# Optimization experiments

Measured on AMD Instinct MI355X. Metric: run time of the kernel, lower is better.

## Reference

```python
import jax, jax.numpy as jnp
import numpy as np

# Geometry constants (from init_kwargs)
H = 512            # volume rows
W = 512            # volume cols
N_ANGLES = 512     # number of projections
N_DET = 736        # detector bins (covers sqrt(2)*512 ~ 724 diagonal)
N_SAMP = 736       # integration samples along each ray
DET_SPACING = 1.0
STEP = 1.0         # ray sampling step (pixel units)


def _bilinear(img, px, py):
    """Bilinear interpolation of img[H,W] at float coords (px=col, py=row); zero outside."""
    x0 = jnp.floor(px)
    y0 = jnp.floor(py)
    fx = px - x0
    fy = py - y0
    x0i = x0.astype(jnp.int32)
    y0i = y0.astype(jnp.int32)

    def tap(yi, xi):
        valid = (xi >= 0) & (xi < W) & (yi >= 0) & (yi < H)
        v = img[jnp.clip(yi, 0, H - 1), jnp.clip(xi, 0, W - 1)]
        return jnp.where(valid, v, jnp.float32(0))

    v00 = tap(y0i, x0i)
    v01 = tap(y0i, x0i + 1)
    v10 = tap(y0i + 1, x0i)
    v11 = tap(y0i + 1, x0i + 1)
    return (v00 * (1 - fx) + v01 * fx) * (1 - fy) + (v10 * (1 - fx) + v11 * fx) * fy


def _parallel_projection2d(img, angles):
    """Parallel-beam Radon transform of img[H,W] -> sinogram [A, N_DET]."""
    cx = (W - 1) * 0.5
    cy = (H - 1) * 0.5
    # detector offsets s and ray-parameter samples t, centered
    s = (jnp.arange(N_DET, dtype=jnp.float32) - (N_DET - 1) * 0.5) * DET_SPACING
    t = (jnp.arange(N_SAMP, dtype=jnp.float32) - (N_SAMP - 1) * 0.5) * STEP

    def project_angle(theta):
        c = jnp.cos(theta)
        si = jnp.sin(theta)
        # ray point = s * (c, si) + t * (-si, c), shifted to image center. [D, T]
        px = s[:, None] * c - t[None, :] * si + cx
        py = s[:, None] * si + t[None, :] * c + cy
        return _bilinear(img, px, py).sum(axis=-1) * STEP  # [D]

    # sequential map over angles keeps intermediates at [D, T] instead of [A, D, T]
    return jax.lax.map(project_angle, angles)  # [A, D]


def setup_inputs() -> dict:
    key = jax.random.key(0)
    k1, k2 = jax.random.split(key)
    x = jax.random.normal(k1, (1, H, W), dtype=jnp.float32)
    # reco variable is constrained non-negative in the original (clip_by_value(x,0,inf))
    reco = jax.random.uniform(k2, (1, H, W), dtype=jnp.float32)
    angles = jnp.linspace(0.0, np.pi, N_ANGLES, endpoint=False, dtype=jnp.float32)
    return {"x": x, "reco": reco, "angles": angles}


def reference(x, reco, angles):
    updated_reco = x + reco                               # [1, H, W]
    sino = jax.vmap(lambda im: _parallel_projection2d(im, angles))(updated_reco)  # [1, A, D]
    return sino, reco
```

## Files before the change

### kernel.cpp

```cpp
#include <hip/hip_runtime.h>
#include <hip/hip_fp16.h>
#include <climits>


namespace {
constexpr int H = 512, W = 512, NA = 512, ND = 736, NS = 736;
constexpr int SINO_SIZE = NA * ND;
constexpr int IMG_SIZE = H * W;
constexpr int QN = 514;
constexpr int QS = 520;
constexpr int QUAD_SIZE = QN * QS;
constexpr int KSPLIT = 8;
}

typedef __fp16 h2 __attribute__((ext_vector_type(2)));
typedef float  f2 __attribute__((ext_vector_type(2)));

__global__ __launch_bounds__(256) void prep_quads(const float* __restrict__ x,
                                                  const float* __restrict__ reco,
                                                  uint2* __restrict__ Q,
                                                  uint2* __restrict__ QT,
                                                  float* __restrict__ reco_out,
                                                  float* __restrict__ sino) {
    __shared__ float tile[34][35];
    const int tx = threadIdx.x, ty = threadIdx.y;
    const int r0 = blockIdx.y * 32, c0 = blockIdx.x * 32;
    const int z  = blockIdx.z;

    if (z == 0) {
        const int nthr = 289 * 256;
        const int gtid = (blockIdx.y * 17 + blockIdx.x) * 256 + ty * 32 + tx;
        for (int i = gtid; i < SINO_SIZE; i += nthr) sino[i] = 0.f;
    }

    for (int li = ty * 32 + tx; li < 34 * 34; li += 256) {
        const int yy = li / 34, xx = li - yy * 34;
        const int r = r0 - 1 + yy, c = c0 - 1 + xx;
        float v = 0.f;
        if ((unsigned)r < 512u && (unsigned)c < 512u) {
            const int i = r * W + c;
            v = x[i] + reco[i];
        }
        tile[yy][xx] = v;
    }
    __syncthreads();

    const int t2 = ty + 8 * z;
    const int ri = r0 + t2, ci = c0 + tx;
    if (ri < QN && ci < QN) {
        uint2 q;
        q.x = __builtin_bit_cast(unsigned int,
              __builtin_amdgcn_cvt_pkrtz(tile[t2][tx],     tile[t2 + 1][tx]));
        q.y = __builtin_bit_cast(unsigned int,
              __builtin_amdgcn_cvt_pkrtz(tile[t2][tx + 1]     - tile[t2][tx],
                                         tile[t2 + 1][tx + 1] - tile[t2 + 1][tx]));
        Q[ri * QS + ci] = q;
    }
    const int ri2 = c0 + t2, ci2 = r0 + tx;
    if (ri2 < QN && ci2 < QN) {
        uint2 q;
        q.x = __builtin_bit_cast(unsigned int,
              __builtin_amdgcn_cvt_pkrtz(tile[tx][t2],     tile[tx][t2 + 1]));
        q.y = __builtin_bit_cast(unsigned int,
              __builtin_amdgcn_cvt_pkrtz(tile[tx + 1][t2]     - tile[tx][t2],
                                         tile[tx + 1][t2 + 1] - tile[tx][t2 + 1]));
        QT[ri2 * QS + ci2] = q;
    }
    const int rr = r0 + t2, cc = c0 + tx;
    if (rr < H && cc < W) reco_out[rr * W + cc] = reco[rr * W + cc];
}

__device__ inline void range1(float p0, float inc, float lo, float hi,
                              float& klo, float& khi) {
    if (inc > 1e-6f)       { klo = (lo - p0) / inc; khi = (hi - p0) / inc; }
    else if (inc < -1e-6f) { klo = (hi - p0) / inc; khi = (lo - p0) / inc; }
    else if (p0 >= lo && p0 <= hi) { klo = -1e9f; khi = 1e9f; }
    else                   { klo = 1e9f;  khi = -1e9f; }
}

__device__ __forceinline__ void samp_clamped(const uint2* __restrict__ base,
                                             float F1, float S1, float fi, float sl,
                                             int j, float& acc) {
    const float jf = (float)j;
    float pf = fmaf(jf, fi, F1);
    float ps = fmaf(jf, sl, S1);
    pf = fminf(fmaxf(pf, 0.f), 513.f);
    ps = fminf(fmaxf(ps, 0.f), 513.f);
    const float ff = floorf(pf), sf = floorf(ps);
    const float fx = pf - ff,   fy = ps - sf;
    const unsigned ai = (unsigned)fmaf(sf, 520.f, ff);
    const uint2 q = base[ai];
    const h2 l  = __builtin_bit_cast(h2, q.x);
    const h2 dl = __builtin_bit_cast(h2, q.y);
    const h2 fxx = __builtin_amdgcn_cvt_pkrtz(fx, fx);
    const h2 m = fxx * dl + l;
    const h2 wy = __builtin_amdgcn_cvt_pkrtz(1.f - fy, fy);
#if __has_builtin(__builtin_amdgcn_fdot2)
    acc = __builtin_amdgcn_fdot2(wy, m, acc, false);
#else
    acc += (float)wy.x * (float)m.x + (float)wy.y * (float)m.y;
#endif
}

__global__ __launch_bounds__(128) void proj_quad(const uint2* __restrict__ Q,
                                                 const uint2* __restrict__ QT,
                                                 const float* __restrict__ angles,
                                                 float* __restrict__ sino) {
    const int lane = threadIdx.x & 63;
    const int d = blockIdx.x * 128 + (threadIdx.x >> 6) * 64 + lane;
    const int a = blockIdx.y;
    const int z = blockIdx.z;

    float si, co;
    sincosf(angles[a], &si, &co);

    const float cx = (W - 1) * 0.5f, cy = (H - 1) * 0.5f;
    const float s  = (float)d - (ND - 1) * 0.5f;
    const float bx = fmaf(s, co, cx);
    const float by = fmaf(s, si, cy);

    const uint2* base;
    float f0, fi, s0, sl, dS;
    if (fabsf(co) >= fabsf(si)) { base = Q;  f0 = bx; fi = -si; s0 = by; sl = co;  dS = si; }
    else                        { base = QT; f0 = by; fi = co;  s0 = bx; sl = -si; dS = co; }

    const float t0 = -(float)(NS - 1) * 0.5f;
    float F0 = fmaf(t0, fi, f0);
    float S0 = fmaf(t0, sl, s0);
    if (sl < 0.f) {
        F0 = fmaf((float)(NS - 1), fi, F0); fi = -fi;
        S0 = fmaf((float)(NS - 1), sl, S0); sl = -sl;
    }

    float kloF, khiF, kloS, khiS;
    range1(F0, fi, -0.9999f, 511.9999f, kloF, khiF);
    range1(S0, sl, -0.9999f, 511.9999f, kloS, khiS);
    const int kA = max(0,      (int)ceilf(fmaxf(kloF, kloS)));
    const int kB = min(NS - 1, (int)floorf(fminf(khiF, khiS)));

    const int o = (int)rintf(-(float)lane * dS / sl);
    const float F1 = fmaf((float)o, fi, F0) + 1.f;
    const float S1 = fmaf((float)o, sl, S0) + 1.f;

    int jA, jB;
    if (kA <= kB) { jA = kA - o; jB = kB - o; }
    else          { jA = INT_MAX; jB = INT_MIN; }
    int Jlo = jA, Jhi = jB;
    #pragma unroll
    for (int off = 1; off < 64; off <<= 1) {
        Jlo = min(Jlo, __shfl_xor(Jlo, off));
        Jhi = max(Jhi, __shfl_xor(Jhi, off));
    }
    if (Jlo > Jhi) return;
    const int L  = Jhi - Jlo + 1;
    const int js = __builtin_amdgcn_readfirstlane(Jlo + (L * z) / KSPLIT);
    const int je = __builtin_amdgcn_readfirstlane(Jlo + (L * (z + 1)) / KSPLIT - 1);
    const int n  = je - js + 1;
    const int je2 = js + 2 * (n >> 1) - 1;

    const f2 fi2 = {fi, fi}, sl2 = {sl, sl};
    const f2 F12 = {F1, F1}, S12 = {S1, S1};
    const f2 c520 = {520.f, 520.f};
    f2 jf2 = {(float)js, (float)(js + 1)};
    float acc0 = 0.f, acc1 = 0.f;
    #pragma unroll 4
    for (int j = js; j <= je2; j += 2) {
        f2 pf = jf2 * fi2 + F12;
        f2 ps = jf2 * sl2 + S12;
        jf2 += (f2)2.f;
        pf = __builtin_elementwise_min(__builtin_elementwise_max(pf, (f2)0.f), (f2)513.f);
        ps = __builtin_elementwise_min(__builtin_elementwise_max(ps, (f2)0.f), (f2)513.f);
        const f2 ff = {__builtin_floorf(pf.x), __builtin_floorf(pf.y)};
        const f2 sf = {__builtin_floorf(ps.x), __builtin_floorf(ps.y)};
        const f2 fx = pf - ff;
        const f2 fy = ps - sf;
        const f2 gy = (f2)1.f - fy;
        const f2 aif = sf * c520 + ff;
        const unsigned a0 = (unsigned)aif.x;
        const unsigned a1 = (unsigned)aif.y;
        const uint2 q0 = base[a0];
        const uint2 q1 = base[a1];
        const h2 fxh = __builtin_amdgcn_cvt_pkrtz(fx.x, fx.y);
        {
            const h2 l   = __builtin_bit_cast(h2, q0.x);
            const h2 dl  = __builtin_bit_cast(h2, q0.y);
            const h2 fxx = {fxh.x, fxh.x};
            const h2 m   = fxx * dl + l;
            const h2 wy  = __builtin_amdgcn_cvt_pkrtz(gy.x, fy.x);
#if __has_builtin(__builtin_amdgcn_fdot2)
            acc0 = __builtin_amdgcn_fdot2(wy, m, acc0, false);
#else
            acc0 += (float)wy.x * (float)m.x + (float)wy.y * (float)m.y;
#endif
        }
        {
            const h2 l   = __builtin_bit_cast(h2, q1.x);
            const h2 dl  = __builtin_bit_cast(h2, q1.y);
            const h2 fxx = {fxh.y, fxh.y};
            const h2 m   = fxx * dl + l;
            const h2 wy  = __builtin_amdgcn_cvt_pkrtz(gy.y, fy.y);
#if __has_builtin(__builtin_amdgcn_fdot2)
            acc1 = __builtin_amdgcn_fdot2(wy, m, acc1, false);
#else
            acc1 += (float)wy.x * (float)m.x + (float)wy.y * (float)m.y;
#endif
        }
    }
    if (n & 1)
        samp_clamped(base, F1, S1, fi, sl, je, acc1);

    const float acc = acc0 + acc1;
    if (d < ND)
        __hip_atomic_fetch_add(&sino[a * ND + d], acc,
                               __ATOMIC_RELAXED, __HIP_MEMORY_SCOPE_AGENT);
}

__global__ __launch_bounds__(256) void proj_fused(const float* __restrict__ A,
                                                  const float* __restrict__ B,
                                                  const float* __restrict__ angles,
                                                  float* __restrict__ sino) {
    const int d = blockIdx.x * blockDim.x + threadIdx.x;
    const int a = blockIdx.y;
    if (d >= ND) return;
    float si, c;
    sincosf(angles[a], &si, &c);
    const float cx = (W - 1) * 0.5f, cy = (H - 1) * 0.5f;
    const float s  = (float)d - (ND - 1) * 0.5f;
    const float bx = fmaf(s, c, cx), by = fmaf(s, si, cy);
    const float t0 = -(float)(NS - 1) * 0.5f;
    float acc = 0.f;
    for (int k = 0; k < NS; ++k) {
        const float t = t0 + (float)k;
        const float px = fmaf(t, -si, bx), py = fmaf(t, c, by);
        const float x0f = floorf(px), y0f = floorf(py);
        const float fx = px - x0f, fy = py - y0f;
        const int ix = (int)x0f, iy = (int)y0f;
        auto tap = [&](int yi, int xi) -> float {
            if (xi < 0 || xi >= W || yi < 0 || yi >= H) return 0.f;
            return A[yi * W + xi] + B[yi * W + xi];
        };
        float v = 0.f;
        if (ix >= -1 && iy >= -1 && ix <= W - 1 && iy <= H - 1) {
            const float v00 = tap(iy, ix),     v01 = tap(iy, ix + 1);
            const float v10 = tap(iy + 1, ix), v11 = tap(iy + 1, ix + 1);
            const float top = fmaf(fx, v01 - v00, v00);
            const float bot = fmaf(fx, v11 - v10, v10);
            v = fmaf(fy, bot - top, top);
        }
        acc += v;
    }
    sino[a * ND + d] = acc;
}

__global__ void prep_copy(const float* __restrict__ reco, float* __restrict__ reco_out) {
    int i = blockIdx.x * blockDim.x + threadIdx.x;
    if (i < IMG_SIZE) reco_out[i] = reco[i];
}

extern "C" void kernel_launch(void* const* d_in, const int* in_sizes, int n_in,
                              void* d_out, int out_size, void* d_ws, size_t ws_size,
                              hipStream_t stream) {
    const float* x      = (const float*)d_in[0];
    const float* reco   = (const float*)d_in[1];
    const float* angles = (const float*)d_in[2];
    float* sino     = (float*)d_out;
    float* reco_out = sino + SINO_SIZE;

    const size_t need_quads = 2 * (size_t)QUAD_SIZE * sizeof(uint2);

    if (ws_size >= need_quads) {
        uint2* Q  = (uint2*)d_ws;
        uint2* QT = Q + QUAD_SIZE;
        prep_quads<<<dim3(17, 17, 4), dim3(32, 8), 0, stream>>>(x, reco, Q, QT, reco_out, sino);
        proj_quad<<<dim3(6, NA, KSPLIT), dim3(128), 0, stream>>>(Q, QT, angles, sino);
    } else {
        prep_copy<<<dim3((IMG_SIZE + 255) / 256), dim3(256), 0, stream>>>(reco, reco_out);
        proj_fused<<<dim3((ND + 255) / 256, NA), dim3(256), 0, stream>>>(x, reco, angles, sino);
    }
}
```

Measured before the change: 147.3 us.

## Precompute sin/cos table, halve K-split, use fast reciprocals and deeper unroll

The prep kernel now writes a per-angle sin/cos table, so the projection blocks read two floats instead of each calling sincosf. Divisions in the ray-range setup and lane offset become hardware reciprocal approximations. The K-split drops from 8 to 4 and the main loop unroll rises from 4 to 8, with a launch-bounds occupancy hint added. Fewer splits cut per-block setup and atomic traffic but lower parallelism, and the approximate reciprocal may shift range endpoints slightly.

```diff
diff --git a/kernel.cpp b/kernel.cpp
--- a/kernel.cpp
+++ b/kernel.cpp
@@ -10,16 +10,26 @@
 constexpr int QN = 514;
 constexpr int QS = 520;
 constexpr int QUAD_SIZE = QN * QS;
-constexpr int KSPLIT = 8;
+constexpr int KSPLIT = 4;
 }
 
 typedef __fp16 h2 __attribute__((ext_vector_type(2)));
 typedef float  f2 __attribute__((ext_vector_type(2)));
+
+__device__ __forceinline__ float fast_rcp(float x) {
+#if __has_builtin(__builtin_amdgcn_rcpf)
+    return __builtin_amdgcn_rcpf(x);
+#else
+    return 1.0f / x;
+#endif
+}
 
 __global__ __launch_bounds__(256) void prep_quads(const float* __restrict__ x,
                                                   const float* __restrict__ reco,
                                                   uint2* __restrict__ Q,
                                                   uint2* __restrict__ QT,
+                                                  const float* __restrict__ angles,
+                                                  float2* __restrict__ sctab,
                                                   float* __restrict__ reco_out,
                                                   float* __restrict__ sino) {
     __shared__ float tile[34][35];
@@ -31,6 +41,14 @@
         const int nthr = 289 * 256;
         const int gtid = (blockIdx.y * 17 + blockIdx.x) * 256 + ty * 32 + tx;
         for (int i = gtid; i < SINO_SIZE; i += nthr) sino[i] = 0.f;
+    }
+    if (z == 1) {
+        const int gtid = (blockIdx.y * 17 + blockIdx.x) * 256 + ty * 32 + tx;
+        if (gtid < NA) {
+            float si, co;
+            sincosf(angles[gtid], &si, &co);
+            sctab[gtid] = make_float2(si, co);
+        }
     }
 
     for (int li = ty * 32 + tx; li < 34 * 34; li += 256) {
@@ -72,10 +90,12 @@
 
 __device__ inline void range1(float p0, float inc, float lo, float hi,
                               float& klo, float& khi) {
-    if (inc > 1e-6f)       { klo = (lo - p0) / inc; khi = (hi - p0) / inc; }
-    else if (inc < -1e-6f) { klo = (hi - p0) / inc; khi = (lo - p0) / inc; }
-    else if (p0 >= lo && p0 <= hi) { klo = -1e9f; khi = 1e9f; }
-    else                   { klo = 1e9f;  khi = -1e9f; }
+    if (fabsf(inc) > 1e-6f) {
+        const float r = fast_rcp(inc);
+        const float a = (lo - p0) * r, b = (hi - p0) * r;
+        klo = fminf(a, b); khi = fmaxf(a, b);
+    } else if (p0 >= lo && p0 <= hi) { klo = -1e9f; khi = 1e9f; }
+    else                             { klo = 1e9f;  khi = -1e9f; }
 }
 
 __device__ __forceinline__ void samp_clamped(const uint2* __restrict__ base,
@@ -102,17 +122,17 @@
 #endif
 }
 
-__global__ __launch_bounds__(128) void proj_quad(const uint2* __restrict__ Q,
-                                                 const uint2* __restrict__ QT,
-                                                 const float* __restrict__ angles,
-                                                 float* __restrict__ sino) {
+__global__ __launch_bounds__(128, 8) void proj_quad(const uint2* __restrict__ Q,
+                                                    const uint2* __restrict__ QT,
+                                                    const float2* __restrict__ sctab,
+                                                    float* __restrict__ sino) {
     const int lane = threadIdx.x & 63;
     const int d = blockIdx.x * 128 + (threadIdx.x >> 6) * 64 + lane;
     const int a = blockIdx.y;
     const int z = blockIdx.z;
 
-    float si, co;
-    sincosf(angles[a], &si, &co);
+    const float2 sc = sctab[a];
+    const float si = sc.x, co = sc.y;
 
     const float cx = (W - 1) * 0.5f, cy = (H - 1) * 0.5f;
     const float s  = (float)d - (ND - 1) * 0.5f;
@@ -138,7 +158,7 @@
     const int kA = max(0,      (int)ceilf(fmaxf(kloF, kloS)));
     const int kB = min(NS - 1, (int)floorf(fminf(khiF, khiS)));
 
-    const int o = (int)rintf(-(float)lane * dS / sl);
+    const int o = (int)rintf(-(float)lane * dS * fast_rcp(sl));
     const float F1 = fmaf((float)o, fi, F0) + 1.f;
     const float S1 = fmaf((float)o, sl, S0) + 1.f;
 
@@ -163,7 +183,7 @@
     const f2 c520 = {520.f, 520.f};
     f2 jf2 = {(float)js, (float)(js + 1)};
     float acc0 = 0.f, acc1 = 0.f;
-    #pragma unroll 4
+    #pragma unroll 8
     for (int j = js; j <= je2; j += 2) {
         f2 pf = jf2 * fi2 + F12;
         f2 ps = jf2 * sl2 + S12;
@@ -266,13 +286,16 @@
     float* sino     = (float*)d_out;
     float* reco_out = sino + SINO_SIZE;
 
-    const size_t need_quads = 2 * (size_t)QUAD_SIZE * sizeof(uint2);
+    const size_t need_quads = 2 * (size_t)QUAD_SIZE * sizeof(uint2)
+                            + (size_t)NA * sizeof(float2);
 
     if (ws_size >= need_quads) {
         uint2* Q  = (uint2*)d_ws;
         uint2* QT = Q + QUAD_SIZE;
-        prep_quads<<<dim3(17, 17, 4), dim3(32, 8), 0, stream>>>(x, reco, Q, QT, reco_out, sino);
-        proj_quad<<<dim3(6, NA, KSPLIT), dim3(128), 0, stream>>>(Q, QT, angles, sino);
+        float2* sctab = (float2*)(QT + QUAD_SIZE);
+        prep_quads<<<dim3(17, 17, 4), dim3(32, 8), 0, stream>>>(x, reco, Q, QT, angles,
+                                                                sctab, reco_out, sino);
+        proj_quad<<<dim3(6, NA, KSPLIT), dim3(128), 0, stream>>>(Q, QT, sctab, sino);
     } else {
         prep_copy<<<dim3((IMG_SIZE + 255) / 256), dim3(256), 0, stream>>>(reco, reco_out);
         proj_fused<<<dim3((ND + 255) / 256, NA), dim3(256), 0, stream>>>(x, reco, angles, sino);
```

Result: slower. 150.6 us (+2.2%).
